# Optimization experiments

Hardware: AMD Instinct MI355X
Metric: run time of the kernel (lower is better)

Reference implementation:

```python
import jax, jax.numpy as jnp
import numpy as np

S, N, LAT, HID, NH, NLAYERS = 8, 128, 128, 384, 8, 6
HT, WT, DT = 128, 128, 128
DIN, DOUT, RAD, LEVELS, FED = 1169, 3 + 3 * 128, 3, 4, 64


def sincos1d(d, pos):
    # MAE-style 1d sincos embedding, d even -> [..., d]
    omega = 1.0 / (10000.0 ** (jnp.arange(d // 2, dtype=jnp.float32) / (d / 2.0)))
    ang = pos[..., None] * omega
    return jnp.concatenate([jnp.sin(ang), jnp.cos(ang)], axis=-1)


def flow_embed(f, Cd=FED):
    # get_3d_embedding(flows, 64, cat_coords=True) -> [..., 3*Cd+3] = 195
    div = jnp.arange(0, Cd, 2, dtype=jnp.float32) * (1000.0 / Cd)
    outs = []
    for a in range(3):
        ang = f[..., a, None] * div
        pe = jnp.stack([jnp.sin(ang), jnp.cos(ang)], axis=-1).reshape(f.shape[:-1] + (Cd,))
        outs.append(pe)
    return jnp.concatenate(outs + [f], axis=-1)


def avg_pool2(x):
    B, Sv, Cc, H, W = x.shape
    return x.reshape(B, Sv, Cc, H // 2, 2, W // 2, 2).mean(axis=(4, 6))


def pyramid(fm):
    pyr = [fm]
    for _ in range(LEVELS - 1):
        fm = avg_pool2(fm)
        pyr.append(fm)
    return pyr


def bilinear_sample(corr, xy):
    # corr: [B,S,N,H,W]; xy: [B,S,N,P,2] pixel coords (x indexes W, y indexes H); zero padding
    B, Sv, Nn, H, W = corr.shape
    cf = corr.reshape(B, Sv, Nn, H * W)
    x, y = xy[..., 0], xy[..., 1]
    x0f = jnp.floor(x); y0f = jnp.floor(y)
    wx, wy = x - x0f, y - y0f
    x0 = x0f.astype(jnp.int32); y0 = y0f.astype(jnp.int32)

    def gather(xi, yi):
        ok = ((xi >= 0) & (xi < W) & (yi >= 0) & (yi < H)).astype(cf.dtype)
        idx = jnp.clip(yi, 0, H - 1) * W + jnp.clip(xi, 0, W - 1)
        v = jnp.take_along_axis(cf, idx.reshape(B, Sv, Nn, -1), axis=-1).reshape(idx.shape)
        return v * ok

    v00 = gather(x0, y0); v01 = gather(x0 + 1, y0)
    v10 = gather(x0, y0 + 1); v11 = gather(x0 + 1, y0 + 1)
    return v00 * (1 - wx) * (1 - wy) + v01 * wx * (1 - wy) + v10 * (1 - wx) * wy + v11 * wx * wy


def corr_sample(pyr, targets, coords):
    # RAFT/CoTracker CorrBlock: per-level dense correlation then (2r+1)^2 window bilinear lookup
    d = jnp.arange(-RAD, RAD + 1, dtype=jnp.float32)
    delta = jnp.stack(jnp.meshgrid(d, d, indexing="ij"), axis=-1).reshape(-1, 2)  # [49,2]
    scale = 1.0 / jnp.sqrt(jnp.float32(targets.shape[-1]))
    outs = []
    for l, fm in enumerate(pyr):
        corr = jnp.einsum("bsnc,bschw->bsnhw", targets, fm) * scale
        xy = coords[..., None, :] / (2.0 ** l) + delta
        outs.append(bilinear_sample(corr, xy))
    return jnp.concatenate(outs, axis=-1)  # [B,S,N,196]


def layernorm(x, g, b):
    m = x.mean(-1, keepdims=True)
    v = x.var(-1, keepdims=True)
    return (x - m) / jnp.sqrt(v + 1e-5) * g + b


def attention(x, Wqkv, bq, Wo, bo):
    M, T, H = x.shape
    dh = H // NH
    qkv = (x @ Wqkv + bq).reshape(M, T, 3, NH, dh)
    q, k, v = qkv[:, :, 0], qkv[:, :, 1], qkv[:, :, 2]
    att = jax.nn.softmax(jnp.einsum("mthd,mshd->mhts", q, k) / jnp.sqrt(jnp.float32(dh)), axis=-1)
    o = jnp.einsum("mhts,mshd->mthd", att, v).reshape(M, T, H)
    return o @ Wo + bo


def updateformer(x, support, W_in, b_in, lnp, Wqkv, bqkv, Wo, bo, W1, b1, W2, b2, W_out, b_out, Ws, bs):
    # x: [B,N,T,DIN]; alternating time (over T) and space (over N) pre-LN transformer blocks
    B, Np, T, _ = x.shape
    sproj = support @ Ws + bs  # [100,HID]
    h = x @ W_in + b_in + sproj.mean(axis=0)
    for i in range(NLAYERS):
        g1, bb1, g2, bb2 = lnp[i, 0], lnp[i, 1], lnp[i, 2], lnp[i, 3]
        if i % 2 == 0:
            y = h.reshape(B * Np, T, HID)
        else:
            y = h.transpose(0, 2, 1, 3).reshape(B * T, Np, HID)
        y = y + attention(layernorm(y, g1, bb1), Wqkv[i], bqkv[i], Wo[i], bo[i])
        z = layernorm(y, g2, bb2)
        y = y + jax.nn.gelu(z @ W1[i] + b1[i], approximate=False) @ W2[i] + b2[i]
        if i % 2 == 0:
            h = y.reshape(B, Np, T, HID)
        else:
            h = y.reshape(B, T, Np, HID).transpose(0, 2, 1, 3)
    return h @ W_out + b_out, sproj[None]


def groupnorm1(x, g, b):
    m = x.mean(-1, keepdims=True)
    v = x.var(-1, keepdims=True)
    return (x - m) / jnp.sqrt(v + 1e-5) * g + b


def _forward(fmapXY, fmapYZ, fmapXZ, coords_init, vis_init, track_mask, feat_init, support_features,
             W_in, b_in, lnp, Wqkv, bqkv, Wo, bo, W1, b1, W2, b2, W_out, b_out, Ws, bs,
             gn_g, gn_b, Wu, bu, Wvis, bvis, iters):
    B, Sv, Cc, H, W = fmapXY.shape
    D = fmapXZ.shape[-2]
    Nn = coords_init.shape[2]
    coords = coords_init
    ffeats = [feat_init[..., k] for k in range(3)]
    pyrXY, pyrYZ, pyrXZ = pyramid(fmapXY), pyramid(fmapYZ), pyramid(fmapXZ)
    grid_size = jnp.array([H, W, D], dtype=jnp.float32)
    # 3d sincos pos embed from query coords; 1169 padded to 1170 -> 390/axis, truncated back
    g = (coords[:, 0] / grid_size * 2.0 - 1.0) * 128.0  # [B,N,3]
    pe = jnp.concatenate([sincos1d(390, g[..., i]) for i in range(3)], axis=-1)[..., :DIN]
    pos_embed = pe.reshape(B * Nn, 1, DIN)
    times_embed = sincos1d(1170, jnp.arange(Sv, dtype=jnp.float32))[None, :, :DIN]
    support = support_features
    for _ in range(iters):
        coords = jax.lax.stop_gradient(coords)  # matches coords.detach()
        fxy = corr_sample(pyrXY, ffeats[0], coords[..., :2])
        fyz = corr_sample(pyrYZ, ffeats[1], coords[..., 1:3])
        fxz = corr_sample(pyrXZ, ffeats[2], coords[..., 0::2])
        fcorrs = jnp.concatenate([fxy, fyz, fxz], axis=-1)  # [B,S,N,588]
        fcorrs_ = fcorrs.transpose(0, 2, 1, 3).reshape(B * Nn, Sv, -1)
        flows_ = (coords - coords[:, :1]).transpose(0, 2, 1, 3).reshape(B * Nn, Sv, 3)
        flows_cat = flow_embed(flows_)  # [BN,S,195]
        ff = [f.transpose(0, 2, 1, 3).reshape(B * Nn, Sv, LAT) for f in ffeats]
        ffeats_ = jnp.concatenate(ff, axis=-1)  # [BN,S,384]
        # replicate torch's cat(dim=2)+permute+reshape layout exactly
        tmv = jnp.concatenate([track_mask, vis_init], axis=2).transpose(0, 2, 1, 3).reshape(B * Nn, Sv, 2)
        tin = jnp.concatenate([flows_cat, fcorrs_, ffeats_, tmv], axis=-1)  # [BN,S,1169]
        x = (tin + pos_embed + times_embed).reshape(B, Nn, Sv, DIN)
        delta, dse3 = updateformer(x, support, W_in, b_in, lnp, Wqkv, bqkv, Wo, bo, W1, b1, W2, b2, W_out, b_out, Ws, bs)
        support = support + dse3[0] / 100.0
        delta = delta.reshape(B * Nn, Sv, DOUT)
        d_coord = delta[..., :3].reshape(B, Nn, Sv, 3).transpose(0, 2, 1, 3)
        coords = coords + d_coord
        new_ffeats = []
        for k in range(3):
            dfk = delta[..., 3 + k * LAT:3 + (k + 1) * LAT]
            upd = jax.nn.gelu(groupnorm1(dfk, gn_g[k], gn_b[k]) @ Wu[k] + bu[k], approximate=False)
            new_ffeats.append(ffeats[k] + upd.reshape(B, Nn, Sv, LAT).transpose(0, 2, 1, 3))
        ffeats = new_ffeats
    vis = (jnp.concatenate(ffeats, axis=-1) @ Wvis + bvis)[..., 0]  # [B,S,N]
    return jnp.concatenate([coords, vis[..., None]], axis=-1)  # [B,S,N,4]


def setup_inputs() -> dict:
    key = jax.random.key(0)
    ks = jax.random.split(key, 16)
    f32 = jnp.float32
    B = 1
    fmapXY = jax.random.normal(ks[0], (B, S, LAT, HT, WT), f32)
    fmapYZ = jax.random.normal(ks[1], (B, S, LAT, DT, HT), f32)
    fmapXZ = jax.random.normal(ks[2], (B, S, LAT, DT, WT), f32)
    coords_init = jax.random.uniform(ks[3], (B, S, N, 3), f32) * 112.0 + 8.0
    vis_init = jnp.ones((B, S, N, 1), f32)
    track_mask = jnp.ones((B, S, N, 1), f32)
    feat_init = jax.random.normal(ks[4], (B, S, N, LAT, 3), f32)
    support_features = jnp.zeros((100, HID), f32) + 0.1
    w = lambda k, sh: jax.random.normal(k, sh, f32) * 0.02
    ln1 = jnp.stack([jnp.ones(HID, f32), jnp.zeros(HID, f32), jnp.ones(HID, f32), jnp.zeros(HID, f32)])
    params = dict(
        W_in=w(ks[5], (DIN, HID)), b_in=jnp.zeros((HID,), f32),
        lnp=jnp.tile(ln1[None], (NLAYERS, 1, 1)),
        Wqkv=w(ks[6], (NLAYERS, HID, 3 * HID)), bqkv=jnp.zeros((NLAYERS, 3 * HID), f32),
        Wo=w(ks[7], (NLAYERS, HID, HID)), bo=jnp.zeros((NLAYERS, HID), f32),
        W1=w(ks[8], (NLAYERS, HID, 4 * HID)), b1=jnp.zeros((NLAYERS, 4 * HID), f32),
        W2=w(ks[9], (NLAYERS, 4 * HID, HID)), b2=jnp.zeros((NLAYERS, HID), f32),
        W_out=w(ks[10], (HID, DOUT)), b_out=jnp.zeros((DOUT,), f32),
        Ws=w(ks[11], (HID, HID)), bs=jnp.zeros((HID,), f32),
        gn_g=jnp.ones((3, LAT), f32), gn_b=jnp.zeros((3, LAT), f32),
        Wu=w(ks[12], (3, LAT, LAT)), bu=jnp.zeros((3, LAT), f32),
        Wvis=w(ks[13], (3 * LAT, 1)), bvis=jnp.zeros((1,), f32),
    )
    return dict(fmapXY=fmapXY, fmapYZ=fmapYZ, fmapXZ=fmapXZ, coords_init=coords_init,
                vis_init=vis_init, track_mask=track_mask, feat_init=feat_init,
                support_features=support_features, iters=2, **params)


def reference(fmapXY, fmapYZ, fmapXZ, coords_init, vis_init, track_mask, feat_init, support_features,
              W_in, b_in, lnp, Wqkv, bqkv, Wo, bo, W1, b1, W2, b2, W_out, b_out, Ws, bs,
              gn_g, gn_b, Wu, bu, Wvis, bvis, iters):
    return _forward(fmapXY, fmapYZ, fmapXZ, coords_init, vis_init, track_mask, feat_init, support_features,
                    W_in, b_in, lnp, Wqkv, bqkv, Wo, bo, W1, b1, W2, b2, W_out, b_out, Ws, bs,
                    gn_g, gn_b, Wu, bu, Wvis, bvis, iters)
```

## Files before the change

kernel.cpp:

```cpp
#include <hip/hip_runtime.h>
#include <hip/hip_bf16.h>


#define DEVFN __device__ __forceinline__

typedef __attribute__((ext_vector_type(8))) short short8;
typedef __attribute__((ext_vector_type(4))) float f32x4;

static constexpr float INV_SQRT_DH = 0.14433756729740643f;
static constexpr float CORR_SCALE  = 0.08838834764831845f;
static constexpr size_t VSTRIDE = 22282240;

DEVFN float gelu_exact(float x){
  return 0.5f * x * (1.0f + erff(x * 0.7071067811865476f));
}
DEVFN short bf16_of(float f){
  __hip_bfloat16 b = __float2bfloat16(f);
  return *reinterpret_cast<short*>(&b);
}
DEVFN float bfu(uint32_t u16){ return __uint_as_float(u16 << 16); }


__global__ void init_state_k(float* coords, const float* cinit,
                             float* ff, const float* feat_init,
                             float* support, const float* sfeat){
  int idx = blockIdx.x*256 + threadIdx.x;
  if (idx < 3072)  coords[idx]  = cinit[idx];
  if (idx < 49152){
    int row = idx / 384;
    support[idx] = (row < 100) ? sfeat[idx] : 0.0f;
  }
  if (idx < 393216){
    int k = idx / 131072, rest = idx % 131072;
    ff[idx] = feat_init[(size_t)rest*3 + k];
  }
}

__global__ void build_posE_k(float* posE, const float* cinit){
  int idx = blockIdx.x*256 + threadIdx.x;
  if (idx >= 128*1169) return;
  int n = idx / 1169, d = idx % 1169;
  int i = d / 390, dd = d % 390;
  float c = cinit[n*3 + i];
  float g = (c / 128.0f * 2.0f - 1.0f) * 128.0f;
  int m = (dd < 195) ? dd : dd - 195;
  float om = powf(10000.0f, -(float)m / 195.0f);
  float ang = g * om;
  posE[idx] = (dd < 195) ? sinf(ang) : cosf(ang);
}

__global__ void build_timE_k(float* timE){
  int idx = blockIdx.x*256 + threadIdx.x;
  if (idx >= 8*1169) return;
  int s = idx / 1169, d = idx % 1169;
  int m = (d < 585) ? d : d - 585;
  float om = powf(10000.0f, -(float)m / 585.0f);
  float ang = (float)s * om;
  timE[idx] = (d < 585) ? sinf(ang) : cosf(ang);
}

__global__ void transpose_cl_k(const float* __restrict__ inXY, const float* __restrict__ inYZ,
                               const float* __restrict__ inXZ, __hip_bfloat16* __restrict__ pyr){
  __shared__ float tile[32][33];
  int v = blockIdx.z >> 3, s = blockIdx.z & 7;
  const float* in = (v==0) ? inXY : ((v==1) ? inYZ : inXZ);
  int c0 = blockIdx.y*32, h0 = blockIdx.x*32;
  int tx = threadIdx.x & 31, ty = threadIdx.x >> 5;
  const float* ib = in + (size_t)s*128*16384;
  #pragma unroll
  for (int r=0;r<4;r++){
    int c = c0 + ty + r*8;
    tile[ty + r*8][tx] = ib[(size_t)c*16384 + h0 + tx];
  }
  __syncthreads();
  __hip_bfloat16* ob = pyr + (size_t)v*VSTRIDE + (size_t)s*16384*128;
  #pragma unroll
  for (int r=0;r<4;r++){
    int hw = h0 + ty + r*8;
    ob[(size_t)hw*128 + c0 + tx] = __float2bfloat16(tile[tx][ty + r*8]);
  }
}

__global__ void pool2_k(__hip_bfloat16* __restrict__ pyr, size_t in_off, size_t out_off, int So){
  int idx = blockIdx.x*256 + threadIdx.x;
  int total = 8*So*So*128;
  if (idx >= total) return;
  const __hip_bfloat16* in = pyr + (size_t)blockIdx.z*VSTRIDE + in_off;
  __hip_bfloat16* out      = pyr + (size_t)blockIdx.z*VSTRIDE + out_off;
  int c = idx & 127;
  int x = (idx >> 7) % So;
  int y = ((idx >> 7) / So) % So;
  int s = idx / (So*So*128);
  int Si = So*2;
  const __hip_bfloat16* b0 = in + (((size_t)s*Si + 2*y)*Si + 2*x)*128 + c;
  float v = __bfloat162float(b0[0]) + __bfloat162float(b0[128])
          + __bfloat162float(b0[(size_t)Si*128]) + __bfloat162float(b0[(size_t)Si*128 + 128]);
  out[idx] = __float2bfloat16(v*0.25f);
}

__global__ void wtrans_k(const float* __restrict__ in, __hip_bfloat16* __restrict__ out,
                         int K, int N, int Kpad, int Npad){
  __shared__ float tile[32][33];
  int z = blockIdx.z;
  const float* ib = in + (size_t)z*K*N;
  __hip_bfloat16* ob = out + (size_t)z*Npad*Kpad;
  int kb = blockIdx.y*32, nb = blockIdx.x*32;
  int tx = threadIdx.x & 31, ty = threadIdx.x >> 5;
  #pragma unroll
  for (int r=0;r<4;r++){
    int k = kb + ty + r*8, n = nb + tx;
    tile[ty+r*8][tx] = (k < K && n < N) ? ib[(size_t)k*N + n] : 0.0f;
  }
  __syncthreads();
  #pragma unroll
  for (int r=0;r<4;r++){
    int n = nb + ty + r*8, k = kb + tx;
    if (n < Npad && k < Kpad) ob[(size_t)n*Kpad + k] = __float2bfloat16(tile[tx][ty+r*8]);
  }
}

__global__ void assemble_x_k(__hip_bfloat16* __restrict__ xbuf, const float* __restrict__ posE,
                             const float* __restrict__ timE, const float* __restrict__ coords,
                             const float* __restrict__ ff, const float* __restrict__ tmask,
                             const float* __restrict__ vinit){
  int r = blockIdx.x;
  int n = r >> 3, s = r & 7;
  for (int d = threadIdx.x; d < 1184; d += blockDim.x){
    __hip_bfloat16* dst = xbuf + (size_t)r*1184 + d;
    if (d >= 1169){ *dst = __float2bfloat16(0.0f); continue; }
    float base = posE[(size_t)n*1169 + d] + timE[(size_t)s*1169 + d];
    if (d >= 195 && d < 783){ *dst = __float2bfloat16(base); continue; }
    float val;
    if (d < 195){
      if (d >= 192){
        int a = d - 192;
        val = coords[(s*128+n)*3 + a] - coords[n*3 + a];
      } else {
        int a = d >> 6, dd = d & 63;
        float f = coords[(s*128+n)*3 + a] - coords[n*3 + a];
        float ang = f * (31.25f * (float)(dd >> 1));
        val = (dd & 1) ? cosf(ang) : sinf(ang);
      }
    } else if (d < 1167){
      int cidx = d - 783, k = cidx >> 7, cc = cidx & 127;
      val = ff[(size_t)k*131072 + (size_t)(s*128+n)*128 + cc];
    } else {
      int c = d - 1167;
      int flat = n*16 + s*2 + c;
      int n2 = flat >> 3, s2 = flat & 7;
      val = (n2 < 128) ? tmask[s2*128 + n2] : vinit[s2*128 + (n2-128)];
    }
    *dst = __float2bfloat16(val + base);
  }
}

__global__ void corr_k(const __hip_bfloat16* __restrict__ pyr, const float* __restrict__ coords,
                       const float* __restrict__ ff, __hip_bfloat16* __restrict__ xbuf){
  __shared__ float t[128];
  __shared__ float p[64];
  int bid = blockIdx.x;
  int view = bid >> 10, s = (bid >> 7) & 7, n = bid & 127;
  int tid = threadIdx.x;
  t[tid]      = ff[(size_t)view*131072 + (size_t)(s*128+n)*128 + tid];
  t[tid + 64] = ff[(size_t)view*131072 + (size_t)(s*128+n)*128 + tid + 64];
  int ax = (view==1) ? 1 : 0;
  int ay = (view==0) ? 1 : 2;
  float X = coords[(s*128+n)*3 + ax];
  float Y = coords[(s*128+n)*3 + ay];
  const __hip_bfloat16* vb = pyr + (size_t)view*VSTRIDE;
  __syncthreads();
  size_t loff = 0;
  for (int l=0;l<4;l++){
    int sz = 128 >> l;
    float inv = 1.0f / (float)(1 << l);
    float cx = X * inv, cy = Y * inv;
    float x0f = floorf(cx), y0f = floorf(cy);
    float wx = cx - x0f, wy = cy - y0f;
    int ix0 = (int)x0f, iy0 = (int)y0f;
    int px = ix0 - 3 + (tid & 7);
    int py = iy0 - 3 + (tid >> 3);
    float acc = 0.0f;
    if (px >= 0 && px < sz && py >= 0 && py < sz){
      const uint2* row = reinterpret_cast<const uint2*>(vb + loff + (((size_t)s*sz + py)*sz + px)*128);
      #pragma unroll
      for (int c4=0;c4<32;c4++){
        uint2 u = row[c4];
        float f0 = __uint_as_float(u.x << 16);
        float f1 = __uint_as_float(u.x & 0xffff0000u);
        float f2 = __uint_as_float(u.y << 16);
        float f3 = __uint_as_float(u.y & 0xffff0000u);
        acc += t[c4*4+0]*f0 + t[c4*4+1]*f1 + t[c4*4+2]*f2 + t[c4*4+3]*f3;
      }
    }
    p[tid] = acc;
    __syncthreads();
    if (tid < 49){
      int i = tid / 7, jj = tid % 7;
      float v = p[jj*8+i]       * (1.0f-wx)*(1.0f-wy)
              + p[jj*8+i+1]     * wx*(1.0f-wy)
              + p[(jj+1)*8+i]   * (1.0f-wx)*wy
              + p[(jj+1)*8+i+1] * wx*wy;
      __hip_bfloat16* dst = xbuf + (size_t)(n*8+s)*1184 + 195 + view*196 + l*49 + tid;
      *dst = __float2bfloat16(__bfloat162float(*dst) + v * CORR_SCALE);
    }
    loff += (size_t)8*sz*sz*128;
    __syncthreads();
  }
}

__global__ void gn_rows_k(const float* __restrict__ dbuf,
                          const float* __restrict__ gn_g, const float* __restrict__ gn_b,
                          __hip_bfloat16* __restrict__ gtmp, float* __restrict__ coords){
  int k = blockIdx.y;
  const float* in = dbuf + 3 + k*128;
  const float* g = gn_g + k*128;
  const float* b = gn_b + k*128;
  __hip_bfloat16* out = gtmp + (size_t)k*131072;
  int wave = threadIdx.x >> 6, lane = threadIdx.x & 63;
  int r = blockIdx.x*4 + wave;
  const float* row = in + (size_t)r*387;
  float x0 = row[lane], x1 = row[lane+64];
  float sum = x0 + x1;
  #pragma unroll
  for (int o=32;o>0;o>>=1) sum += __shfl_xor(sum, o);
  float mean = sum / 128.0f;
  float d0 = x0-mean, d1 = x1-mean;
  float vs = d0*d0 + d1*d1;
  #pragma unroll
  for (int o=32;o>0;o>>=1) vs += __shfl_xor(vs, o);
  float invstd = 1.0f / sqrtf(vs/128.0f + 1e-5f);
  out[(size_t)r*128 + lane]      = __float2bfloat16(d0*invstd*g[lane] + b[lane]);
  out[(size_t)r*128 + lane + 64] = __float2bfloat16(d1*invstd*g[lane+64] + b[lane+64]);
  if (k == 0 && blockIdx.x < 12){
    int idx = blockIdx.x*256 + threadIdx.x;
    if (idx < 3072){
      int a = idx % 3, sn = idx / 3;
      int ss = sn >> 7, nn = sn & 127;
      coords[idx] += dbuf[(size_t)(nn*8+ss)*387 + a];
    }
  }
}

template<int K, int MODE, bool AF32>
__global__ __launch_bounds__(256) void mgemm_k(const void* __restrict__ A, int lda,
                                               const __hip_bfloat16* __restrict__ Bt,
                                               float* __restrict__ C, int ldc,
                                               int M, int N,
                                               const float* __restrict__ bias){
  constexpr int NSTEP = K/32;
  int tid = threadIdx.x;
  int lane = tid & 63, wid = tid >> 6;
  int wr = wid >> 1, wc = wid & 1;
  int lr = lane & 15, lk = lane >> 4;
  int m0 = blockIdx.y*64 + wr*32;
  int n0 = blockIdx.x*64 + wc*32;

  const __hip_bfloat16* Ab = (const __hip_bfloat16*)A;
  const float* Af = (const float*)A;
  size_t arow0 = (size_t)(m0 + lr)      * lda;
  size_t arow1 = (size_t)(m0 + 16 + lr) * lda;
  size_t brow0 = (size_t)(n0 + lr)      * K;
  size_t brow1 = (size_t)(n0 + 16 + lr) * K;

  auto loadA = [&](size_t ro, int k0)->short8{
    if constexpr (AF32){
      const float* p = Af + ro + k0 + lk*8;
      short8 r;
      #pragma unroll
      for (int j=0;j<8;j++) r[j] = bf16_of(p[j]);
      return r;
    } else {
      return *reinterpret_cast<const short8*>(Ab + ro + k0 + lk*8);
    }
  };
  auto loadB = [&](size_t ro, int k0)->short8{
    return *reinterpret_cast<const short8*>(Bt + ro + k0 + lk*8);
  };

  short8 a0[3], a1[3], b0[3], b1[3];
  #pragma unroll
  for (int p=0;p<3;p++){
    if (p < NSTEP){
      a0[p]=loadA(arow0,p*32); a1[p]=loadA(arow1,p*32);
      b0[p]=loadB(brow0,p*32); b1[p]=loadB(brow1,p*32);
    }
  }
  f32x4 acc00 = {}, acc01 = {}, acc10 = {}, acc11 = {};
  #pragma unroll
  for (int t=0;t<NSTEP;t++){
    const int cur = t % 3;
    acc00 = __builtin_amdgcn_mfma_f32_16x16x32_bf16(a0[cur],b0[cur],acc00,0,0,0);
    acc01 = __builtin_amdgcn_mfma_f32_16x16x32_bf16(a0[cur],b1[cur],acc01,0,0,0);
    acc10 = __builtin_amdgcn_mfma_f32_16x16x32_bf16(a1[cur],b0[cur],acc10,0,0,0);
    acc11 = __builtin_amdgcn_mfma_f32_16x16x32_bf16(a1[cur],b1[cur],acc11,0,0,0);
    if (t+3 < NSTEP){
      int k0 = (t+3)*32;
      a0[cur]=loadA(arow0,k0); a1[cur]=loadA(arow1,k0);
      b0[cur]=loadB(brow0,k0); b1[cur]=loadB(brow1,k0);
    }
  }

  f32x4 accs[2][2] = {{acc00, acc01},{acc10, acc11}};
  #pragma unroll
  for (int mi=0;mi<2;mi++){
    #pragma unroll
    for (int ni=0;ni<2;ni++){
      int c = n0 + ni*16 + lr;
      if (c >= N) continue;
      float bv = bias ? bias[c] : 0.0f;
      #pragma unroll
      for (int reg=0;reg<4;reg++){
        int r = m0 + mi*16 + lk*4 + reg;
        if (r >= M) continue;
        float v = accs[mi][ni][reg] + bv;
        if (MODE==0) C[(size_t)r*ldc + c] = v;
        else C[(size_t)r*ldc + c] += v;
      }
    }
  }
}

template<bool GELU>
__global__ __launch_bounds__(256) void lngemm_k(const float* __restrict__ A,
                                                const float* __restrict__ gamma,
                                                const float* __restrict__ beta,
                                                const __hip_bfloat16* __restrict__ Bt,
                                                __hip_bfloat16* __restrict__ Cbf, int ldc,
                                                const float* __restrict__ bias){
  constexpr int LDSS = 392;
  __shared__ short Asm[64*LDSS];
  int tid = threadIdx.x, lane = tid & 63, w = tid >> 6;
  int m0 = blockIdx.y*64, n0b = blockIdx.x*128;

  float gg[6], bb[6];
  #pragma unroll
  for (int e=0;e<6;e++){ gg[e] = gamma[lane+e*64]; bb[e] = beta[lane+e*64]; }
  for (int rr=0; rr<16; rr++){
    int r = w*16 + rr;
    const float* row = A + (size_t)(m0+r)*384;
    float x[6]; float sum = 0.0f;
    #pragma unroll
    for (int e=0;e<6;e++){ x[e] = row[lane+e*64]; sum += x[e]; }
    #pragma unroll
    for (int o=32;o>0;o>>=1) sum += __shfl_xor(sum, o);
    float mean = sum * (1.0f/384.0f);
    float vs = 0.0f;
    #pragma unroll
    for (int e=0;e<6;e++){ float d = x[e]-mean; vs += d*d; }
    #pragma unroll
    for (int o=32;o>0;o>>=1) vs += __shfl_xor(vs, o);
    float invstd = 1.0f / sqrtf(vs*(1.0f/384.0f) + 1e-5f);
    #pragma unroll
    for (int e=0;e<6;e++)
      Asm[r*LDSS + lane + e*64] = bf16_of((x[e]-mean)*invstd*gg[e] + bb[e]);
  }
  __syncthreads();

  int wr = w >> 1, wc = w & 1;
  int lr = lane & 15, lk = lane >> 4;
  const __hip_bfloat16* Brow[4];
  #pragma unroll
  for (int ni=0;ni<4;ni++) Brow[ni] = Bt + (size_t)(n0b + wc*64 + ni*16 + lr)*384;

  short8 bfrag[2][4];
  #pragma unroll
  for (int p=0;p<2;p++)
    #pragma unroll
    for (int ni=0;ni<4;ni++)
      bfrag[p][ni] = *(const short8*)(Brow[ni] + p*32 + lk*8);

  f32x4 acc[2][4] = {};
  #pragma unroll
  for (int t=0;t<12;t++){
    const int cur = t & 1;
    short8 a0 = *(const short8*)(&Asm[(wr*32+lr)*LDSS    + t*32 + lk*8]);
    short8 a1 = *(const short8*)(&Asm[(wr*32+16+lr)*LDSS + t*32 + lk*8]);
    #pragma unroll
    for (int ni=0;ni<4;ni++){
      acc[0][ni] = __builtin_amdgcn_mfma_f32_16x16x32_bf16(a0,bfrag[cur][ni],acc[0][ni],0,0,0);
      acc[1][ni] = __builtin_amdgcn_mfma_f32_16x16x32_bf16(a1,bfrag[cur][ni],acc[1][ni],0,0,0);
    }
    if (t+2 < 12){
      #pragma unroll
      for (int ni=0;ni<4;ni++)
        bfrag[cur][ni] = *(const short8*)(Brow[ni] + (t+2)*32 + lk*8);
    }
  }
  #pragma unroll
  for (int mi=0;mi<2;mi++){
    #pragma unroll
    for (int ni=0;ni<4;ni++){
      int c = n0b + wc*64 + ni*16 + lr;
      float bv = bias[c];
      #pragma unroll
      for (int reg=0;reg<4;reg++){
        int r = m0 + wr*32 + mi*16 + lk*4 + reg;
        float v = acc[mi][ni][reg] + bv;
        Cbf[(size_t)r*ldc + c] = __float2bfloat16(GELU ? gelu_exact(v) : v);
      }
    }
  }
}

__global__ __launch_bounds__(256) void wu_gemm_k(const __hip_bfloat16* __restrict__ gtmp,
                                                 const __hip_bfloat16* __restrict__ WuT,
                                                 const float* __restrict__ bu,
                                                 float* __restrict__ ff){
  int z = blockIdx.z;
  const __hip_bfloat16* A  = gtmp + (size_t)z*131072;
  const __hip_bfloat16* Bt = WuT  + (size_t)z*16384;
  const float* bias = bu + (size_t)z*128;
  float* aux = ff + (size_t)z*131072;
  int tid = threadIdx.x, lane = tid & 63, wid = tid >> 6;
  int wr = wid >> 1, wc = wid & 1;
  int lr = lane & 15, lk = lane >> 4;
  int m0 = blockIdx.y*64 + wr*32;
  int n0 = blockIdx.x*64 + wc*32;
  const short8* A0 = (const short8*)(A + (size_t)(m0+lr)*128);
  const short8* A1 = (const short8*)(A + (size_t)(m0+16+lr)*128);
  const short8* B0 = (const short8*)(Bt + (size_t)(n0+lr)*128);
  const short8* B1 = (const short8*)(Bt + (size_t)(n0+16+lr)*128);
  f32x4 acc00={}, acc01={}, acc10={}, acc11={};
  #pragma unroll
  for (int t=0;t<4;t++){
    short8 a0 = A0[t*4 + lk], a1 = A1[t*4 + lk];
    short8 b0 = B0[t*4 + lk], b1 = B1[t*4 + lk];
    acc00 = __builtin_amdgcn_mfma_f32_16x16x32_bf16(a0,b0,acc00,0,0,0);
    acc01 = __builtin_amdgcn_mfma_f32_16x16x32_bf16(a0,b1,acc01,0,0,0);
    acc10 = __builtin_amdgcn_mfma_f32_16x16x32_bf16(a1,b0,acc10,0,0,0);
    acc11 = __builtin_amdgcn_mfma_f32_16x16x32_bf16(a1,b1,acc11,0,0,0);
  }
  f32x4 accs[2][2] = {{acc00, acc01},{acc10, acc11}};
  #pragma unroll
  for (int mi=0;mi<2;mi++){
    #pragma unroll
    for (int ni=0;ni<2;ni++){
      int c = n0 + ni*16 + lr;
      float bv = bias[c];
      #pragma unroll
      for (int reg=0;reg<4;reg++){
        int r = m0 + mi*16 + lk*4 + reg;
        float v = accs[mi][ni][reg] + bv;
        int ss = r & 7, nn2 = r >> 3;
        aux[((size_t)(ss*128+nn2))*128 + c] += gelu_exact(v);
      }
    }
  }
}

__global__ __launch_bounds__(512) void attn_even_k(const __hip_bfloat16* __restrict__ qkv,
                                                   __hip_bfloat16* __restrict__ attout){
  int g = blockIdx.x;
  int h = threadIdx.x >> 6;
  int lane = threadIdx.x & 63;
  int t = lane >> 3, j = lane & 7;
  const short* qs = (const short*)qkv;

  float q[48], kk[48];
  {
    const short8* qp = (const short8*)(qs + (size_t)(g*8+t)*1152 + h*48);
    const short8* kp = (const short8*)(qs + (size_t)(g*8+j)*1152 + 384 + h*48);
    #pragma unroll
    for (int c=0;c<6;c++){
      short8 qv = qp[c], kv = kp[c];
      #pragma unroll
      for (int e=0;e<8;e++){
        q[c*8+e]  = bfu((uint16_t)qv[e]);
        kk[c*8+e] = bfu((uint16_t)kv[e]);
      }
    }
  }
  float s = 0.0f;
  #pragma unroll
  for (int d=0;d<48;d++) s += q[d]*kk[d];
  s *= INV_SQRT_DH;
  float mx = s;
  #pragma unroll
  for (int o=1;o<8;o<<=1) mx = fmaxf(mx, __shfl_xor(mx, o));
  float e = expf(s - mx);
  float l = e;
  #pragma unroll
  for (int o=1;o<8;o<<=1) l += __shfl_xor(l, o);
  float p = e / l;

  float o6[6] = {0,0,0,0,0,0};
  #pragma unroll
  for (int jp=0;jp<8;jp++){
    float pj = __shfl(p, (lane & 56) | jp);
    const uint32_t* vp = (const uint32_t*)(qs + (size_t)(g*8+jp)*1152 + 768 + h*48 + j*6);
    uint32_t w0 = vp[0], w1 = vp[1], w2 = vp[2];
    o6[0] += pj * bfu(w0 & 0xffffu); o6[1] += pj * bfu(w0 >> 16);
    o6[2] += pj * bfu(w1 & 0xffffu); o6[3] += pj * bfu(w1 >> 16);
    o6[4] += pj * bfu(w2 & 0xffffu); o6[5] += pj * bfu(w2 >> 16);
  }
  uint32_t r0 = ((uint32_t)(uint16_t)bf16_of(o6[1]) << 16) | (uint16_t)bf16_of(o6[0]);
  uint32_t r1 = ((uint32_t)(uint16_t)bf16_of(o6[3]) << 16) | (uint16_t)bf16_of(o6[2]);
  uint32_t r2 = ((uint32_t)(uint16_t)bf16_of(o6[5]) << 16) | (uint16_t)bf16_of(o6[4]);
  uint32_t* op = (uint32_t*)((short*)attout + (size_t)(g*8+t)*384 + h*48 + j*6);
  op[0] = r0; op[1] = r1; op[2] = r2;
}

__global__ __launch_bounds__(256) void attn_odd_mfma_k(const __hip_bfloat16* __restrict__ qkv,
                                                       __hip_bfloat16* __restrict__ attout){
  __shared__ char smem[47872];
  short* Qb = (short*)smem;
  short* Kb = (short*)(smem + 18432);
  short* Pb = (short*)smem;
  short* Vt = (short*)(smem + 34816);
  int g = blockIdx.x & 7, h = blockIdx.x >> 3;
  int tid = threadIdx.x;

  const short* qs = (const short*)qkv;
  for (int idx = tid; idx < 768; idx += 256){
    int t = idx / 6, dblk = idx % 6;
    size_t base = (size_t)(t*8+g)*1152 + h*48 + dblk*8;
    *(short8*)(Qb + t*72 + dblk*8) = *(const short8*)(qs + base);
    *(short8*)(Kb + t*72 + dblk*8) = *(const short8*)(qs + base + 384);
  }
  short8 zz = {};
  for (int idx = tid; idx < 384; idx += 256){
    int t = idx / 3, dblk = idx % 3;
    *(short8*)(Qb + t*72 + 48 + dblk*8) = zz;
    *(short8*)(Kb + t*72 + 48 + dblk*8) = zz;
  }
  __syncthreads();

  int lane = tid & 63, w = tid >> 6;
  int lr = lane & 15, lk = lane >> 4;
  int m0 = w*32;

  f32x4 S[2][8] = {};
  #pragma unroll
  for (int ks=0; ks<2; ks++){
    short8 a0 = *(const short8*)(Qb + (m0+lr)*72    + ks*32 + lk*8);
    short8 a1 = *(const short8*)(Qb + (m0+16+lr)*72 + ks*32 + lk*8);
    #pragma unroll
    for (int ni=0; ni<8; ni++){
      short8 b = *(const short8*)(Kb + (ni*16+lr)*72 + ks*32 + lk*8);
      S[0][ni] = __builtin_amdgcn_mfma_f32_16x16x32_bf16(a0,b,S[0][ni],0,0,0);
      S[1][ni] = __builtin_amdgcn_mfma_f32_16x16x32_bf16(a1,b,S[1][ni],0,0,0);
    }
  }

  #pragma unroll
  for (int mi=0;mi<2;mi++){
    #pragma unroll
    for (int reg=0;reg<4;reg++){
      float m = -1e30f;
      #pragma unroll
      for (int ni=0;ni<8;ni++) m = fmaxf(m, S[mi][ni][reg]);
      #pragma unroll
      for (int o=1;o<16;o<<=1) m = fmaxf(m, __shfl_xor(m, o));
      m *= INV_SQRT_DH;
      float l = 0.0f;
      #pragma unroll
      for (int ni=0;ni<8;ni++){
        float p = expf(S[mi][ni][reg]*INV_SQRT_DH - m);
        S[mi][ni][reg] = p;
        l += p;
      }
      #pragma unroll
      for (int o=1;o<16;o<<=1) l += __shfl_xor(l, o);
      float inv = 1.0f/l;
      #pragma unroll
      for (int ni=0;ni<8;ni++) S[mi][ni][reg] *= inv;
    }
  }
  __syncthreads();

  for (int idx = tid; idx < 768; idx += 256){
    int j = idx / 6, dblk = idx % 6;
    short8 v = *(const short8*)(qs + (size_t)(j*8+g)*1152 + 768 + h*48 + dblk*8);
    #pragma unroll
    for (int e=0;e<8;e++) Vt[(dblk*8+e)*136 + j] = v[e];
  }
  #pragma unroll
  for (int mi=0;mi<2;mi++)
    #pragma unroll
    for (int ni=0;ni<8;ni++)
      #pragma unroll
      for (int reg=0;reg<4;reg++)
        Pb[(m0+mi*16+lk*4+reg)*136 + ni*16+lr] = bf16_of(S[mi][ni][reg]);
  __syncthreads();

  f32x4 O[2][3] = {};
  #pragma unroll
  for (int ks=0; ks<4; ks++){
    short8 a0 = *(const short8*)(Pb + (m0+lr)*136    + ks*32 + lk*8);
    short8 a1 = *(const short8*)(Pb + (m0+16+lr)*136 + ks*32 + lk*8);
    #pragma unroll
    for (int ni=0; ni<3; ni++){
      short8 b = *(const short8*)(Vt + (ni*16+lr)*136 + ks*32 + lk*8);
      O[0][ni] = __builtin_amdgcn_mfma_f32_16x16x32_bf16(a0,b,O[0][ni],0,0,0);
      O[1][ni] = __builtin_amdgcn_mfma_f32_16x16x32_bf16(a1,b,O[1][ni],0,0,0);
    }
  }
  #pragma unroll
  for (int mi=0;mi<2;mi++){
    #pragma unroll
    for (int ni=0;ni<3;ni++){
      #pragma unroll
      for (int reg=0;reg<4;reg++){
        int q = m0 + mi*16 + lk*4 + reg;
        int d = ni*16 + lr;
        attout[(size_t)(q*8+g)*384 + h*48 + d] = __float2bfloat16(O[mi][ni][reg]);
      }
    }
  }
}

__global__ void supp_smean_k(const float* __restrict__ sproj, const float* __restrict__ b_in,
                             float* __restrict__ bias2, float* __restrict__ support){
  int idx = blockIdx.x*256 + threadIdx.x;
  if (idx < 38400) support[idx] += sproj[idx]*0.01f;
  else if (idx < 38784){
    int c = idx - 38400;
    float s = 0.0f;
    for (int r=0;r<100;r++) s += sproj[r*384 + c];
    bias2[c] = b_in[c] + s*0.01f;
  }
}

__global__ void final_out_k(const float* __restrict__ coords, const float* __restrict__ ff,
                            const float* __restrict__ Wvis, const float* __restrict__ bvis,
                            float* __restrict__ out){
  int sn = blockIdx.x*64 + threadIdx.x;
  if (sn >= 1024) return;
  float acc = bvis[0];
  for (int k=0;k<3;k++)
    for (int c=0;c<128;c++)
      acc += ff[(size_t)k*131072 + (size_t)sn*128 + c] * Wvis[k*128 + c];
  out[sn*4+0] = coords[sn*3+0];
  out[sn*4+1] = coords[sn*3+1];
  out[sn*4+2] = coords[sn*3+2];
  out[sn*4+3] = acc;
}


extern "C" void kernel_launch(void* const* d_in, const int* in_sizes, int n_in,
                              void* d_out, int out_size, void* d_ws, size_t ws_size,
                              hipStream_t stream) {
  const float* fmapXY   = (const float*)d_in[0];
  const float* fmapYZ   = (const float*)d_in[1];
  const float* fmapXZ   = (const float*)d_in[2];
  const float* cinit    = (const float*)d_in[3];
  const float* vinit    = (const float*)d_in[4];
  const float* tmask    = (const float*)d_in[5];
  const float* feat_init= (const float*)d_in[6];
  const float* sfeat    = (const float*)d_in[7];
  const float* W_in     = (const float*)d_in[9];
  const float* b_in     = (const float*)d_in[10];
  const float* lnp      = (const float*)d_in[11];
  const float* Wqkv     = (const float*)d_in[12];
  const float* bqkv     = (const float*)d_in[13];
  const float* Wo       = (const float*)d_in[14];
  const float* bo       = (const float*)d_in[15];
  const float* W1       = (const float*)d_in[16];
  const float* b1       = (const float*)d_in[17];
  const float* W2       = (const float*)d_in[18];
  const float* b2       = (const float*)d_in[19];
  const float* W_out    = (const float*)d_in[20];
  const float* b_out    = (const float*)d_in[21];
  const float* Ws       = (const float*)d_in[22];
  const float* bs       = (const float*)d_in[23];
  const float* gn_g     = (const float*)d_in[24];
  const float* gn_b     = (const float*)d_in[25];
  const float* Wu       = (const float*)d_in[26];
  const float* bu       = (const float*)d_in[27];
  const float* Wvis     = (const float*)d_in[28];
  const float* bvis     = (const float*)d_in[29];
  const int ITERS = 2;

  char* wp = (char*)d_ws;
  auto alloc = [&](size_t bytes)->char* {
    char* p = wp; wp += (bytes + 255) & ~(size_t)255; return p;
  };
  __hip_bfloat16* pyr = (__hip_bfloat16*)alloc(3ull*VSTRIDE*2);
  float* coords = (float*)alloc(3072ull*4);
  float* ff     = (float*)alloc(393216ull*4);
  float* support= (float*)alloc(49152ull*4);
  float* sproj  = (float*)alloc(38400ull*4);
  float* bias2  = (float*)alloc(384ull*4);
  float* posE   = (float*)alloc(149632ull*4);
  float* timE   = (float*)alloc(9352ull*4);
  float* h      = (float*)alloc(393216ull*4);
  float* dbuf   = (float*)alloc(396288ull*4);
  __hip_bfloat16* xbuf_bf = (__hip_bfloat16*)alloc(1212416ull*2);
  __hip_bfloat16* qkv_bf  = (__hip_bfloat16*)alloc(1179648ull*2);
  __hip_bfloat16* atto_bf = (__hip_bfloat16*)alloc(393216ull*2);
  __hip_bfloat16* ffb_bf  = (__hip_bfloat16*)alloc(1572864ull*2);
  __hip_bfloat16* gtmp_bf = (__hip_bfloat16*)alloc(393216ull*2);
  __hip_bfloat16* WsT   = (__hip_bfloat16*)alloc(147456ull*2);
  __hip_bfloat16* WinT  = (__hip_bfloat16*)alloc(454656ull*2);
  __hip_bfloat16* WqkvT = (__hip_bfloat16*)alloc(2654208ull*2);
  __hip_bfloat16* WoT   = (__hip_bfloat16*)alloc(884736ull*2);
  __hip_bfloat16* W1T   = (__hip_bfloat16*)alloc(3538944ull*2);
  __hip_bfloat16* W2T   = (__hip_bfloat16*)alloc(3538944ull*2);
  __hip_bfloat16* WoutT = (__hip_bfloat16*)alloc(172032ull*2);
  __hip_bfloat16* WuT   = (__hip_bfloat16*)alloc(49152ull*2);
  if ((size_t)(wp - (char*)d_ws) > ws_size) return;

  init_state_k<<<1536, 256, 0, stream>>>(coords, cinit, ff, feat_init, support, sfeat);
  build_posE_k<<<(128*1169 + 255)/256, 256, 0, stream>>>(posE, cinit);
  build_timE_k<<<(8*1169 + 255)/256, 256, 0, stream>>>(timE);

  transpose_cl_k<<<dim3(512,4,24), 256, 0, stream>>>(fmapXY, fmapYZ, fmapXZ, pyr);
  pool2_k<<<dim3((8*64*64*128 + 255)/256,1,3), 256, 0, stream>>>(pyr, 0,        16777216, 64);
  pool2_k<<<dim3((8*32*32*128 + 255)/256,1,3), 256, 0, stream>>>(pyr, 16777216, 20971520, 32);
  pool2_k<<<dim3((8*16*16*128 + 255)/256,1,3), 256, 0, stream>>>(pyr, 20971520, 22020096, 16);

  wtrans_k<<<dim3(12,12,1), 256, 0, stream>>>(Ws,    WsT,   384, 384, 384, 384);
  wtrans_k<<<dim3(12,37,1), 256, 0, stream>>>(W_in,  WinT,  1169,384, 1184,384);
  wtrans_k<<<dim3(36,12,6), 256, 0, stream>>>(Wqkv,  WqkvT, 384, 1152,384, 1152);
  wtrans_k<<<dim3(12,12,6), 256, 0, stream>>>(Wo,    WoT,   384, 384, 384, 384);
  wtrans_k<<<dim3(48,12,6), 256, 0, stream>>>(W1,    W1T,   384, 1536,384, 1536);
  wtrans_k<<<dim3(12,48,6), 256, 0, stream>>>(W2,    W2T,   1536,384, 1536,384);
  wtrans_k<<<dim3(14,12,1), 256, 0, stream>>>(W_out, WoutT, 384, 387, 384, 448);
  wtrans_k<<<dim3(4,4,3),   256, 0, stream>>>(Wu,    WuT,   128, 128, 128, 128);

  for (int it=0; it<ITERS; ++it){
    assemble_x_k<<<1024, 256, 0, stream>>>(xbuf_bf, posE, timE, coords, ff, tmask, vinit);
    corr_k<<<3072, 64, 0, stream>>>(pyr, coords, ff, xbuf_bf);

    mgemm_k<384,0,true><<<dim3(6,2), 256, 0, stream>>>(support,384, WsT, sproj,384, 100,384, bs);
    supp_smean_k<<<152, 256, 0, stream>>>(sproj, b_in, bias2, support);

    mgemm_k<1184,0,false><<<dim3(6,16), 256, 0, stream>>>(xbuf_bf,1184, WinT, h,384, 1024,384, bias2);

    for (int i=0;i<6;i++){
      const float* g1  = lnp + (size_t)(i*4+0)*384;
      const float* bb1 = lnp + (size_t)(i*4+1)*384;
      const float* g2  = lnp + (size_t)(i*4+2)*384;
      const float* bb2 = lnp + (size_t)(i*4+3)*384;

      lngemm_k<false><<<dim3(9,16), 256, 0, stream>>>(h, g1, bb1, WqkvT + (size_t)i*442368,
                                                      qkv_bf, 1152, bqkv + i*1152);
      if ((i & 1) == 0) attn_even_k<<<128, 512, 0, stream>>>(qkv_bf, atto_bf);
      else              attn_odd_mfma_k<<<64, 256, 0, stream>>>(qkv_bf, atto_bf);
      mgemm_k<384,1,false><<<dim3(6,16), 256, 0, stream>>>(atto_bf,384, WoT + (size_t)i*147456,
                                                           h,384, 1024,384, bo + i*384);
      lngemm_k<true><<<dim3(12,16), 256, 0, stream>>>(h, g2, bb2, W1T + (size_t)i*589824,
                                                      ffb_bf, 1536, b1 + i*1536);
      mgemm_k<1536,1,false><<<dim3(6,16), 256, 0, stream>>>(ffb_bf,1536, W2T + (size_t)i*589824,
                                                            h,384, 1024,384, b2 + i*384);
    }

    mgemm_k<384,0,true><<<dim3(7,16), 256, 0, stream>>>(h,384, WoutT, dbuf,387, 1024,387, b_out);
    gn_rows_k<<<dim3(256,3), 256, 0, stream>>>(dbuf, gn_g, gn_b, gtmp_bf, coords);
    wu_gemm_k<<<dim3(2,16,3), 256, 0, stream>>>(gtmp_bf, WuT, bu, ff);
  }

  final_out_k<<<16, 64, 0, stream>>>(coords, ff, Wvis, bvis, (float*)d_out);
}
```

Measured before the change: 1.459 ms.

## Fuse setup kernels, Wo+LN+W1, and output head; deepen GEMM prefetch

Merges the init, positional-embedding, pooling and weight-transpose launches into single kernels. The pyramid pooling now reads level 0 directly for every level, and the transpose tile is widened to use float4 loads. Per layer, the Wo projection, residual add, LayerNorm and W1 GELU GEMM become one kernel with ping-pong h buffers, and the output head, GroupNorm and Wu update are fused. Prefetch depth rises in mgemm and the LN GEMMs. These changes cut launch count and round-trips through global memory, but each W1 block recomputes the full Wo GEMM for its row tile, and the coarser pooling reads more data.

After: 2.211 ms. +51.6%, slower.

```diff
diff --git a/kernel.cpp b/kernel.cpp
--- a/kernel.cpp
+++ b/kernel.cpp
@@ -19,11 +19,16 @@
   return *reinterpret_cast<short*>(&b);
 }
 DEVFN float bfu(uint32_t u16){ return __uint_as_float(u16 << 16); }
-
-
-__global__ void init_state_k(float* coords, const float* cinit,
-                             float* ff, const float* feat_init,
-                             float* support, const float* sfeat){
+DEVFN float bf2f(__hip_bfloat16 b){ return __bfloat162float(b); }
+
+DEVFN f32x4 MFMA(short8 a, short8 b, f32x4 c){
+  return __builtin_amdgcn_mfma_f32_16x16x32_bf16(a,b,c,0,0,0);
+}
+
+__global__ void init_all_k(float* coords, const float* cinit,
+                           float* ff, const float* feat_init,
+                           float* support, const float* sfeat,
+                           float* posE, float* timE){
   int idx = blockIdx.x*256 + threadIdx.x;
   if (idx < 3072)  coords[idx]  = cinit[idx];
   if (idx < 49152){
@@ -34,88 +39,99 @@
     int k = idx / 131072, rest = idx % 131072;
     ff[idx] = feat_init[(size_t)rest*3 + k];
   }
-}
-
-__global__ void build_posE_k(float* posE, const float* cinit){
-  int idx = blockIdx.x*256 + threadIdx.x;
-  if (idx >= 128*1169) return;
-  int n = idx / 1169, d = idx % 1169;
-  int i = d / 390, dd = d % 390;
-  float c = cinit[n*3 + i];
-  float g = (c / 128.0f * 2.0f - 1.0f) * 128.0f;
-  int m = (dd < 195) ? dd : dd - 195;
-  float om = powf(10000.0f, -(float)m / 195.0f);
-  float ang = g * om;
-  posE[idx] = (dd < 195) ? sinf(ang) : cosf(ang);
-}
-
-__global__ void build_timE_k(float* timE){
-  int idx = blockIdx.x*256 + threadIdx.x;
-  if (idx >= 8*1169) return;
-  int s = idx / 1169, d = idx % 1169;
-  int m = (d < 585) ? d : d - 585;
-  float om = powf(10000.0f, -(float)m / 585.0f);
-  float ang = (float)s * om;
-  timE[idx] = (d < 585) ? sinf(ang) : cosf(ang);
+  if (idx < 149632){
+    int n = idx / 1169, d = idx % 1169;
+    int i = d / 390, dd = d % 390;
+    float c = cinit[n*3 + i];
+    float g = (c / 128.0f * 2.0f - 1.0f) * 128.0f;
+    int m = (dd < 195) ? dd : dd - 195;
+    float om = powf(10000.0f, -(float)m / 195.0f);
+    float ang = g * om;
+    posE[idx] = (dd < 195) ? sinf(ang) : cosf(ang);
+  }
+  if (idx < 9352){
+    int s = idx / 1169, d = idx % 1169;
+    int m = (d < 585) ? d : d - 585;
+    float om = powf(10000.0f, -(float)m / 585.0f);
+    float ang = (float)s * om;
+    timE[idx] = (d < 585) ? sinf(ang) : cosf(ang);
+  }
 }
 
 __global__ void transpose_cl_k(const float* __restrict__ inXY, const float* __restrict__ inYZ,
                                const float* __restrict__ inXZ, __hip_bfloat16* __restrict__ pyr){
-  __shared__ float tile[32][33];
+  __shared__ float tile[32][129];
   int v = blockIdx.z >> 3, s = blockIdx.z & 7;
   const float* in = (v==0) ? inXY : ((v==1) ? inYZ : inXZ);
-  int c0 = blockIdx.y*32, h0 = blockIdx.x*32;
+  int c0 = blockIdx.y*32, h0 = blockIdx.x*128;
   int tx = threadIdx.x & 31, ty = threadIdx.x >> 5;
   const float* ib = in + (size_t)s*128*16384;
   #pragma unroll
   for (int r=0;r<4;r++){
     int c = c0 + ty + r*8;
-    tile[ty + r*8][tx] = ib[(size_t)c*16384 + h0 + tx];
+    float4 f = *reinterpret_cast<const float4*>(ib + (size_t)c*16384 + h0 + tx*4);
+    tile[ty+r*8][tx*4+0]=f.x; tile[ty+r*8][tx*4+1]=f.y;
+    tile[ty+r*8][tx*4+2]=f.z; tile[ty+r*8][tx*4+3]=f.w;
   }
   __syncthreads();
   __hip_bfloat16* ob = pyr + (size_t)v*VSTRIDE + (size_t)s*16384*128;
   #pragma unroll
-  for (int r=0;r<4;r++){
-    int hw = h0 + ty + r*8;
-    ob[(size_t)hw*128 + c0 + tx] = __float2bfloat16(tile[tx][ty + r*8]);
-  }
-}
-
-__global__ void pool2_k(__hip_bfloat16* __restrict__ pyr, size_t in_off, size_t out_off, int So){
+  for (int rr=0;rr<16;rr++){
+    int hw = ty + rr*8;
+    ob[(size_t)(h0+hw)*128 + c0 + tx] = __float2bfloat16(tile[tx][hw]);
+  }
+}
+
+__global__ void pool_all_k(__hip_bfloat16* __restrict__ pyr){
   int idx = blockIdx.x*256 + threadIdx.x;
-  int total = 8*So*So*128;
-  if (idx >= total) return;
-  const __hip_bfloat16* in = pyr + (size_t)blockIdx.z*VSTRIDE + in_off;
-  __hip_bfloat16* out      = pyr + (size_t)blockIdx.z*VSTRIDE + out_off;
-  int c = idx & 127;
-  int x = (idx >> 7) % So;
-  int y = ((idx >> 7) / So) % So;
-  int s = idx / (So*So*128);
-  int Si = So*2;
-  const __hip_bfloat16* b0 = in + (((size_t)s*Si + 2*y)*Si + 2*x)*128 + c;
-  float v = __bfloat162float(b0[0]) + __bfloat162float(b0[128])
-          + __bfloat162float(b0[(size_t)Si*128]) + __bfloat162float(b0[(size_t)Si*128 + 128]);
-  out[idx] = __float2bfloat16(v*0.25f);
-}
-
-__global__ void wtrans_k(const float* __restrict__ in, __hip_bfloat16* __restrict__ out,
-                         int K, int N, int Kpad, int Npad){
+  if (idx >= 5505024) return;
+  const __hip_bfloat16* L0 = pyr + (size_t)blockIdx.z*VSTRIDE;
+  int i = idx, So, F; size_t off;
+  if (i < 4194304){ So=64; F=2; off=16777216; }
+  else if (i < 5242880){ i -= 4194304; So=32; F=4; off=20971520; }
+  else { i -= 5242880; So=16; F=8; off=22020096; }
+  int c = i & 127;
+  int x = (i >> 7) % So;
+  int y = ((i >> 7) / So) % So;
+  int s = i / (So*So*128);
+  float acc = 0.0f;
+  for (int dy=0;dy<F;dy++)
+    for (int dx=0;dx<F;dx++)
+      acc += bf2f(L0[(((size_t)s*128 + y*F+dy)*128 + (x*F+dx))*128 + c]);
+  pyr[(size_t)blockIdx.z*VSTRIDE + off + i] = __float2bfloat16(acc / (float)(F*F));
+}
+
+__global__ void wtrans_all_k(const float* Ws, const float* W_in, const float* Wqkv,
+                             const float* Wo, const float* W1, const float* W2,
+                             const float* W_out, const float* Wu,
+                             __hip_bfloat16* WsT, __hip_bfloat16* WinT, __hip_bfloat16* WqkvT,
+                             __hip_bfloat16* WoT, __hip_bfloat16* W1T, __hip_bfloat16* W2T,
+                             __hip_bfloat16* WoutT, __hip_bfloat16* WuT){
   __shared__ float tile[32][33];
   int z = blockIdx.z;
-  const float* ib = in + (size_t)z*K*N;
-  __hip_bfloat16* ob = out + (size_t)z*Npad*Kpad;
+  const float* in; __hip_bfloat16* out; int K,N,Kp,Np;
+  if (z==0){ in=Ws; out=WsT; K=384;N=384;Kp=384;Np=384; }
+  else if (z==1){ in=W_in; out=WinT; K=1169;N=384;Kp=1184;Np=384; }
+  else if (z<8){ int l=z-2; in=Wqkv+(size_t)l*442368; out=WqkvT+(size_t)l*442368; K=384;N=1152;Kp=384;Np=1152; }
+  else if (z<14){ int l=z-8; in=Wo+(size_t)l*147456; out=WoT+(size_t)l*147456; K=384;N=384;Kp=384;Np=384; }
+  else if (z<20){ int l=z-14; in=W1+(size_t)l*589824; out=W1T+(size_t)l*589824; K=384;N=1536;Kp=384;Np=1536; }
+  else if (z<26){ int l=z-20; in=W2+(size_t)l*589824; out=W2T+(size_t)l*589824; K=1536;N=384;Kp=1536;Np=384; }
+  else if (z==26){ in=W_out; out=WoutT; K=384;N=387;Kp=384;Np=448; }
+  else { int l=z-27; in=Wu+(size_t)l*16384; out=WuT+(size_t)l*16384; K=128;N=128;Kp=128;Np=128; }
+  int MK = (K>Kp)?K:Kp, MN = (N>Np)?N:Np;
   int kb = blockIdx.y*32, nb = blockIdx.x*32;
+  if (kb >= MK || nb >= MN) return;
   int tx = threadIdx.x & 31, ty = threadIdx.x >> 5;
   #pragma unroll
   for (int r=0;r<4;r++){
     int k = kb + ty + r*8, n = nb + tx;
-    tile[ty+r*8][tx] = (k < K && n < N) ? ib[(size_t)k*N + n] : 0.0f;
+    tile[ty+r*8][tx] = (k < K && n < N) ? in[(size_t)k*N + n] : 0.0f;
   }
   __syncthreads();
   #pragma unroll
   for (int r=0;r<4;r++){
     int n = nb + ty + r*8, k = kb + tx;
-    if (n < Npad && k < Kpad) ob[(size_t)n*Kpad + k] = __float2bfloat16(tile[tx][ty+r*8]);
+    if (n < Np && k < Kp) out[(size_t)n*Kp + k] = __float2bfloat16(tile[tx][ty+r*8]);
   }
 }
 
@@ -208,40 +224,7 @@
   }
 }
 
-__global__ void gn_rows_k(const float* __restrict__ dbuf,
-                          const float* __restrict__ gn_g, const float* __restrict__ gn_b,
-                          __hip_bfloat16* __restrict__ gtmp, float* __restrict__ coords){
-  int k = blockIdx.y;
-  const float* in = dbuf + 3 + k*128;
-  const float* g = gn_g + k*128;
-  const float* b = gn_b + k*128;
-  __hip_bfloat16* out = gtmp + (size_t)k*131072;
-  int wave = threadIdx.x >> 6, lane = threadIdx.x & 63;
-  int r = blockIdx.x*4 + wave;
-  const float* row = in + (size_t)r*387;
-  float x0 = row[lane], x1 = row[lane+64];
-  float sum = x0 + x1;
-  #pragma unroll
-  for (int o=32;o>0;o>>=1) sum += __shfl_xor(sum, o);
-  float mean = sum / 128.0f;
-  float d0 = x0-mean, d1 = x1-mean;
-  float vs = d0*d0 + d1*d1;
-  #pragma unroll
-  for (int o=32;o>0;o>>=1) vs += __shfl_xor(vs, o);
-  float invstd = 1.0f / sqrtf(vs/128.0f + 1e-5f);
-  out[(size_t)r*128 + lane]      = __float2bfloat16(d0*invstd*g[lane] + b[lane]);
-  out[(size_t)r*128 + lane + 64] = __float2bfloat16(d1*invstd*g[lane+64] + b[lane+64]);
-  if (k == 0 && blockIdx.x < 12){
-    int idx = blockIdx.x*256 + threadIdx.x;
-    if (idx < 3072){
-      int a = idx % 3, sn = idx / 3;
-      int ss = sn >> 7, nn = sn & 127;
-      coords[idx] += dbuf[(size_t)(nn*8+ss)*387 + a];
-    }
-  }
-}
-
-template<int K, int MODE, bool AF32>
+template<int K, int MODE, bool AF32, int DEPTH>
 __global__ __launch_bounds__(256) void mgemm_k(const void* __restrict__ A, int lda,
                                                const __hip_bfloat16* __restrict__ Bt,
                                                float* __restrict__ C, int ldc,
@@ -277,9 +260,9 @@
     return *reinterpret_cast<const short8*>(Bt + ro + k0 + lk*8);
   };
 
-  short8 a0[3], a1[3], b0[3], b1[3];
-  #pragma unroll
-  for (int p=0;p<3;p++){
+  short8 a0[DEPTH], a1[DEPTH], b0[DEPTH], b1[DEPTH];
+  #pragma unroll
+  for (int p=0;p<DEPTH;p++){
     if (p < NSTEP){
       a0[p]=loadA(arow0,p*32); a1[p]=loadA(arow1,p*32);
       b0[p]=loadB(brow0,p*32); b1[p]=loadB(brow1,p*32);
@@ -288,13 +271,13 @@
   f32x4 acc00 = {}, acc01 = {}, acc10 = {}, acc11 = {};
   #pragma unroll
   for (int t=0;t<NSTEP;t++){
-    const int cur = t % 3;
-    acc00 = __builtin_amdgcn_mfma_f32_16x16x32_bf16(a0[cur],b0[cur],acc00,0,0,0);
-    acc01 = __builtin_amdgcn_mfma_f32_16x16x32_bf16(a0[cur],b1[cur],acc01,0,0,0);
-    acc10 = __builtin_amdgcn_mfma_f32_16x16x32_bf16(a1[cur],b0[cur],acc10,0,0,0);
-    acc11 = __builtin_amdgcn_mfma_f32_16x16x32_bf16(a1[cur],b1[cur],acc11,0,0,0);
-    if (t+3 < NSTEP){
-      int k0 = (t+3)*32;
+    const int cur = t % DEPTH;
+    acc00 = MFMA(a0[cur],b0[cur],acc00);
+    acc01 = MFMA(a0[cur],b1[cur],acc01);
+    acc10 = MFMA(a1[cur],b0[cur],acc10);
+    acc11 = MFMA(a1[cur],b1[cur],acc11);
+    if (t+DEPTH < NSTEP){
+      int k0 = (t+DEPTH)*32;
       a0[cur]=loadA(arow0,k0); a1[cur]=loadA(arow1,k0);
       b0[cur]=loadB(brow0,k0); b1[cur]=loadB(brow1,k0);
     }
@@ -320,12 +303,11 @@
   }
 }
 
-template<bool GELU>
-__global__ __launch_bounds__(256) void lngemm_k(const float* __restrict__ A,
+__global__ __launch_bounds__(256) void ln_qkv_k(const float* __restrict__ A,
                                                 const float* __restrict__ gamma,
                                                 const float* __restrict__ beta,
                                                 const __hip_bfloat16* __restrict__ Bt,
-                                                __hip_bfloat16* __restrict__ Cbf, int ldc,
+                                                __hip_bfloat16* __restrict__ Cbf,
                                                 const float* __restrict__ bias){
   constexpr int LDSS = 392;
   __shared__ short Asm[64*LDSS];
@@ -362,9 +344,9 @@
   #pragma unroll
   for (int ni=0;ni<4;ni++) Brow[ni] = Bt + (size_t)(n0b + wc*64 + ni*16 + lr)*384;
 
-  short8 bfrag[2][4];
-  #pragma unroll
-  for (int p=0;p<2;p++)
+  short8 bfrag[4][4];
+  #pragma unroll
+  for (int p=0;p<4;p++)
     #pragma unroll
     for (int ni=0;ni<4;ni++)
       bfrag[p][ni] = *(const short8*)(Brow[ni] + p*32 + lk*8);
@@ -372,18 +354,18 @@
   f32x4 acc[2][4] = {};
   #pragma unroll
   for (int t=0;t<12;t++){
-    const int cur = t & 1;
+    const int cur = t & 3;
     short8 a0 = *(const short8*)(&Asm[(wr*32+lr)*LDSS    + t*32 + lk*8]);
     short8 a1 = *(const short8*)(&Asm[(wr*32+16+lr)*LDSS + t*32 + lk*8]);
     #pragma unroll
     for (int ni=0;ni<4;ni++){
-      acc[0][ni] = __builtin_amdgcn_mfma_f32_16x16x32_bf16(a0,bfrag[cur][ni],acc[0][ni],0,0,0);
-      acc[1][ni] = __builtin_amdgcn_mfma_f32_16x16x32_bf16(a1,bfrag[cur][ni],acc[1][ni],0,0,0);
-    }
-    if (t+2 < 12){
+      acc[0][ni] = MFMA(a0,bfrag[cur][ni],acc[0][ni]);
+      acc[1][ni] = MFMA(a1,bfrag[cur][ni],acc[1][ni]);
+    }
+    if (t+4 < 12){
       #pragma unroll
       for (int ni=0;ni<4;ni++)
-        bfrag[cur][ni] = *(const short8*)(Brow[ni] + (t+2)*32 + lk*8);
+        bfrag[cur][ni] = *(const short8*)(Brow[ni] + (t+4)*32 + lk*8);
     }
   }
   #pragma unroll
@@ -395,52 +377,235 @@
       #pragma unroll
       for (int reg=0;reg<4;reg++){
         int r = m0 + wr*32 + mi*16 + lk*4 + reg;
-        float v = acc[mi][ni][reg] + bv;
-        Cbf[(size_t)r*ldc + c] = __float2bfloat16(GELU ? gelu_exact(v) : v);
+        Cbf[(size_t)r*1152 + c] = __float2bfloat16(acc[mi][ni][reg] + bv);
       }
     }
   }
 }
 
-__global__ __launch_bounds__(256) void wu_gemm_k(const __hip_bfloat16* __restrict__ gtmp,
-                                                 const __hip_bfloat16* __restrict__ WuT,
-                                                 const float* __restrict__ bu,
-                                                 float* __restrict__ ff){
-  int z = blockIdx.z;
-  const __hip_bfloat16* A  = gtmp + (size_t)z*131072;
-  const __hip_bfloat16* Bt = WuT  + (size_t)z*16384;
-  const float* bias = bu + (size_t)z*128;
+__global__ __launch_bounds__(256) void wo_ln_w1_k(const __hip_bfloat16* __restrict__ atto,
+                                                  const __hip_bfloat16* __restrict__ WoT,
+                                                  const float* __restrict__ bo,
+                                                  const float* __restrict__ hin,
+                                                  float* __restrict__ hout,
+                                                  const float* __restrict__ gamma,
+                                                  const float* __restrict__ beta,
+                                                  const __hip_bfloat16* __restrict__ W1T,
+                                                  const float* __restrict__ b1,
+                                                  __hip_bfloat16* __restrict__ ffb){
+  constexpr int LDSS = 392;
+  __shared__ short Asm[64*LDSS];
+  int tid = threadIdx.x, lane = tid & 63, w = tid >> 6;
+  int lr = lane & 15, lk = lane >> 4;
+  int m0 = blockIdx.y*64;
+
+  f32x4 acc[24];
+  #pragma unroll
+  for (int nt=0;nt<24;nt++) acc[nt] = (f32x4){0.f,0.f,0.f,0.f};
+  const __hip_bfloat16* Arow = atto + (size_t)(m0 + w*16 + lr)*384;
+  #pragma unroll
+  for (int t=0;t<12;t++){
+    short8 a = *(const short8*)(Arow + t*32 + lk*8);
+    #pragma unroll
+    for (int nt=0;nt<24;nt++){
+      short8 b = *(const short8*)(WoT + (size_t)(nt*16+lr)*384 + t*32 + lk*8);
+      acc[nt] = MFMA(a,b,acc[nt]);
+    }
+  }
+  int rbase = m0 + w*16 + lk*4;
+  float sum[4] = {0,0,0,0}, sq[4] = {0,0,0,0};
+  #pragma unroll
+  for (int nt=0;nt<24;nt++){
+    int c = nt*16 + lr;
+    float bv = bo[c];
+    #pragma unroll
+    for (int reg=0;reg<4;reg++){
+      float v = acc[nt][reg] + hin[(size_t)(rbase+reg)*384 + c] + bv;
+      acc[nt][reg] = v;
+      sum[reg] += v; sq[reg] += v*v;
+    }
+  }
+  if (blockIdx.x == 0){
+    #pragma unroll
+    for (int nt=0;nt<24;nt++){
+      int c = nt*16 + lr;
+      #pragma unroll
+      for (int reg=0;reg<4;reg++)
+        hout[(size_t)(rbase+reg)*384 + c] = acc[nt][reg];
+    }
+  }
+  #pragma unroll
+  for (int reg=0;reg<4;reg++){
+    #pragma unroll
+    for (int o=1;o<16;o<<=1){
+      sum[reg] += __shfl_xor(sum[reg], o);
+      sq[reg]  += __shfl_xor(sq[reg], o);
+    }
+  }
+  #pragma unroll
+  for (int reg=0;reg<4;reg++){
+    float mean = sum[reg]*(1.0f/384.0f);
+    float var  = sq[reg]*(1.0f/384.0f) - mean*mean;
+    float inv  = 1.0f / sqrtf(var + 1e-5f);
+    int rloc = w*16 + lk*4 + reg;
+    #pragma unroll
+    for (int nt=0;nt<24;nt++){
+      int c = nt*16 + lr;
+      Asm[rloc*LDSS + c] = bf16_of((acc[nt][reg]-mean)*inv*gamma[c] + beta[c]);
+    }
+  }
+  __syncthreads();
+
+  int wr = w >> 1, wc = w & 1;
+  int n0b = blockIdx.x*128;
+  const __hip_bfloat16* Brow[4];
+  #pragma unroll
+  for (int ni=0;ni<4;ni++) Brow[ni] = W1T + (size_t)(n0b + wc*64 + ni*16 + lr)*384;
+  short8 bfrag[4][4];
+  #pragma unroll
+  for (int p=0;p<4;p++)
+    #pragma unroll
+    for (int ni=0;ni<4;ni++)
+      bfrag[p][ni] = *(const short8*)(Brow[ni] + p*32 + lk*8);
+  f32x4 acc2[2][4] = {};
+  #pragma unroll
+  for (int t=0;t<12;t++){
+    const int cur = t & 3;
+    short8 a0 = *(const short8*)(&Asm[(wr*32+lr)*LDSS    + t*32 + lk*8]);
+    short8 a1 = *(const short8*)(&Asm[(wr*32+16+lr)*LDSS + t*32 + lk*8]);
+    #pragma unroll
+    for (int ni=0;ni<4;ni++){
+      acc2[0][ni] = MFMA(a0,bfrag[cur][ni],acc2[0][ni]);
+      acc2[1][ni] = MFMA(a1,bfrag[cur][ni],acc2[1][ni]);
+    }
+    if (t+4 < 12){
+      #pragma unroll
+      for (int ni=0;ni<4;ni++)
+        bfrag[cur][ni] = *(const short8*)(Brow[ni] + (t+4)*32 + lk*8);
+    }
+  }
+  #pragma unroll
+  for (int mi=0;mi<2;mi++){
+    #pragma unroll
+    for (int ni=0;ni<4;ni++){
+      int c = n0b + wc*64 + ni*16 + lr;
+      float bv = b1[c];
+      #pragma unroll
+      for (int reg=0;reg<4;reg++){
+        int r = m0 + wr*32 + mi*16 + lk*4 + reg;
+        ffb[(size_t)r*1536 + c] = __float2bfloat16(gelu_exact(acc2[mi][ni][reg] + bv));
+      }
+    }
+  }
+}
+
+__global__ void coords_k(float* __restrict__ coords, const float* __restrict__ h,
+                         const __hip_bfloat16* __restrict__ WoutT, const float* __restrict__ b_out){
+  int idx = blockIdx.x*64 + threadIdx.x;
+  if (idx >= 3072) return;
+  int a = idx % 3, sn = idx / 3;
+  int s = sn >> 7, n = sn & 127;
+  const float* hr = h + (size_t)(n*8+s)*384;
+  const __hip_bfloat16* wr = WoutT + (size_t)a*384;
+  float p0=0,p1=0,p2=0,p3=0;
+  for (int k=0;k<384;k+=4){
+    p0 += hr[k  ]*bf2f(wr[k  ]);
+    p1 += hr[k+1]*bf2f(wr[k+1]);
+    p2 += hr[k+2]*bf2f(wr[k+2]);
+    p3 += hr[k+3]*bf2f(wr[k+3]);
+  }
+  coords[idx] += (p0+p1)+(p2+p3) + b_out[a];
+}
+
+__global__ __launch_bounds__(256) void wout_gn_wu_k(const float* __restrict__ h,
+                                                    const __hip_bfloat16* __restrict__ WoutT,
+                                                    const float* __restrict__ b_out,
+                                                    const float* __restrict__ gn_g,
+                                                    const float* __restrict__ gn_b,
+                                                    const __hip_bfloat16* __restrict__ WuT,
+                                                    const float* __restrict__ bu,
+                                                    float* __restrict__ ff){
+  __shared__ short Asm[64*136];
+  int tid = threadIdx.x, lane = tid & 63, w = tid >> 6;
+  int lr = lane & 15, lk = lane >> 4;
+  int m0 = blockIdx.x*64;
+  int z = blockIdx.y;
+
+  f32x4 acc[8];
+  #pragma unroll
+  for (int nt=0;nt<8;nt++) acc[nt] = (f32x4){0.f,0.f,0.f,0.f};
+  const float* Arow = h + (size_t)(m0 + w*16 + lr)*384;
+  #pragma unroll
+  for (int t=0;t<12;t++){
+    short8 a;
+    const float* p = Arow + t*32 + lk*8;
+    #pragma unroll
+    for (int j=0;j<8;j++) a[j] = bf16_of(p[j]);
+    #pragma unroll
+    for (int nt=0;nt<8;nt++){
+      short8 b = *(const short8*)(WoutT + (size_t)(3 + z*128 + nt*16+lr)*384 + t*32 + lk*8);
+      acc[nt] = MFMA(a,b,acc[nt]);
+    }
+  }
+  float sum[4] = {0,0,0,0}, sq[4] = {0,0,0,0};
+  #pragma unroll
+  for (int nt=0;nt<8;nt++){
+    int cc = nt*16 + lr;
+    float bv = b_out[3 + z*128 + cc];
+    #pragma unroll
+    for (int reg=0;reg<4;reg++){
+      float v = acc[nt][reg] + bv;
+      acc[nt][reg] = v;
+      sum[reg] += v; sq[reg] += v*v;
+    }
+  }
+  #pragma unroll
+  for (int reg=0;reg<4;reg++){
+    #pragma unroll
+    for (int o=1;o<16;o<<=1){
+      sum[reg] += __shfl_xor(sum[reg], o);
+      sq[reg]  += __shfl_xor(sq[reg], o);
+    }
+  }
+  #pragma unroll
+  for (int reg=0;reg<4;reg++){
+    float mean = sum[reg]*(1.0f/128.0f);
+    float var  = sq[reg]*(1.0f/128.0f) - mean*mean;
+    float inv  = 1.0f / sqrtf(var + 1e-5f);
+    int rloc = w*16 + lk*4 + reg;
+    #pragma unroll
+    for (int nt=0;nt<8;nt++){
+      int cc = nt*16 + lr;
+      Asm[rloc*136 + cc] = bf16_of((acc[nt][reg]-mean)*inv*gn_g[z*128+cc] + gn_b[z*128+cc]);
+    }
+  }
+  __syncthreads();
+
+  int wr = w >> 1, wc = w & 1;
+  const __hip_bfloat16* Bt = WuT + (size_t)z*16384;
+  f32x4 acc2[2][4] = {};
+  #pragma unroll
+  for (int t=0;t<4;t++){
+    short8 a0 = *(const short8*)(&Asm[(wr*32+lr)*136    + t*32 + lk*8]);
+    short8 a1 = *(const short8*)(&Asm[(wr*32+16+lr)*136 + t*32 + lk*8]);
+    #pragma unroll
+    for (int ni=0;ni<4;ni++){
+      short8 b = *(const short8*)(Bt + (size_t)(wc*64 + ni*16+lr)*128 + t*32 + lk*8);
+      acc2[0][ni] = MFMA(a0,b,acc2[0][ni]);
+      acc2[1][ni] = MFMA(a1,b,acc2[1][ni]);
+    }
+  }
   float* aux = ff + (size_t)z*131072;
-  int tid = threadIdx.x, lane = tid & 63, wid = tid >> 6;
-  int wr = wid >> 1, wc = wid & 1;
-  int lr = lane & 15, lk = lane >> 4;
-  int m0 = blockIdx.y*64 + wr*32;
-  int n0 = blockIdx.x*64 + wc*32;
-  const short8* A0 = (const short8*)(A + (size_t)(m0+lr)*128);
-  const short8* A1 = (const short8*)(A + (size_t)(m0+16+lr)*128);
-  const short8* B0 = (const short8*)(Bt + (size_t)(n0+lr)*128);
-  const short8* B1 = (const short8*)(Bt + (size_t)(n0+16+lr)*128);
-  f32x4 acc00={}, acc01={}, acc10={}, acc11={};
-  #pragma unroll
-  for (int t=0;t<4;t++){
-    short8 a0 = A0[t*4 + lk], a1 = A1[t*4 + lk];
-    short8 b0 = B0[t*4 + lk], b1 = B1[t*4 + lk];
-    acc00 = __builtin_amdgcn_mfma_f32_16x16x32_bf16(a0,b0,acc00,0,0,0);
-    acc01 = __builtin_amdgcn_mfma_f32_16x16x32_bf16(a0,b1,acc01,0,0,0);
-    acc10 = __builtin_amdgcn_mfma_f32_16x16x32_bf16(a1,b0,acc10,0,0,0);
-    acc11 = __builtin_amdgcn_mfma_f32_16x16x32_bf16(a1,b1,acc11,0,0,0);
-  }
-  f32x4 accs[2][2] = {{acc00, acc01},{acc10, acc11}};
   #pragma unroll
   for (int mi=0;mi<2;mi++){
     #pragma unroll
-    for (int ni=0;ni<2;ni++){
-      int c = n0 + ni*16 + lr;
-      float bv = bias[c];
+    for (int ni=0;ni<4;ni++){
+      int c = wc*64 + ni*16 + lr;
+      float bv = bu[z*128 + c];
       #pragma unroll
       for (int reg=0;reg<4;reg++){
-        int r = m0 + mi*16 + lk*4 + reg;
-        float v = accs[mi][ni][reg] + bv;
+        int r = m0 + wr*32 + mi*16 + lk*4 + reg;
+        float v = acc2[mi][ni][reg] + bv;
         int ss = r & 7, nn2 = r >> 3;
         aux[((size_t)(ss*128+nn2))*128 + c] += gelu_exact(v);
       }
@@ -537,8 +702,8 @@
     #pragma unroll
     for (int ni=0; ni<8; ni++){
       short8 b = *(const short8*)(Kb + (ni*16+lr)*72 + ks*32 + lk*8);
-      S[0][ni] = __builtin_amdgcn_mfma_f32_16x16x32_bf16(a0,b,S[0][ni],0,0,0);
-      S[1][ni] = __builtin_amdgcn_mfma_f32_16x16x32_bf16(a1,b,S[1][ni],0,0,0);
+      S[0][ni] = MFMA(a0,b,S[0][ni]);
+      S[1][ni] = MFMA(a1,b,S[1][ni]);
     }
   }
 
@@ -591,8 +756,8 @@
     #pragma unroll
     for (int ni=0; ni<3; ni++){
       short8 b = *(const short8*)(Vt + (ni*16+lr)*136 + ks*32 + lk*8);
-      O[0][ni] = __builtin_amdgcn_mfma_f32_16x16x32_bf16(a0,b,O[0][ni],0,0,0);
-      O[1][ni] = __builtin_amdgcn_mfma_f32_16x16x32_bf16(a1,b,O[1][ni],0,0,0);
+      O[0][ni] = MFMA(a0,b,O[0][ni]);
+      O[1][ni] = MFMA(a1,b,O[1][ni]);
     }
   }
   #pragma unroll
@@ -683,13 +848,12 @@
   float* bias2  = (float*)alloc(384ull*4);
   float* posE   = (float*)alloc(149632ull*4);
   float* timE   = (float*)alloc(9352ull*4);
-  float* h      = (float*)alloc(393216ull*4);
-  float* dbuf   = (float*)alloc(396288ull*4);
+  float* h0buf  = (float*)alloc(393216ull*4);
+  float* h1buf  = (float*)alloc(393216ull*4);
   __hip_bfloat16* xbuf_bf = (__hip_bfloat16*)alloc(1212416ull*2);
   __hip_bfloat16* qkv_bf  = (__hip_bfloat16*)alloc(1179648ull*2);
   __hip_bfloat16* atto_bf = (__hip_bfloat16*)alloc(393216ull*2);
   __hip_bfloat16* ffb_bf  = (__hip_bfloat16*)alloc(1572864ull*2);
-  __hip_bfloat16* gtmp_bf = (__hip_bfloat16*)alloc(393216ull*2);
   __hip_bfloat16* WsT   = (__hip_bfloat16*)alloc(147456ull*2);
   __hip_bfloat16* WinT  = (__hip_bfloat16*)alloc(454656ull*2);
   __hip_bfloat16* WqkvT = (__hip_bfloat16*)alloc(2654208ull*2);
@@ -700,54 +864,43 @@
   __hip_bfloat16* WuT   = (__hip_bfloat16*)alloc(49152ull*2);
   if ((size_t)(wp - (char*)d_ws) > ws_size) return;
 
-  init_state_k<<<1536, 256, 0, stream>>>(coords, cinit, ff, feat_init, support, sfeat);
-  build_posE_k<<<(128*1169 + 255)/256, 256, 0, stream>>>(posE, cinit);
-  build_timE_k<<<(8*1169 + 255)/256, 256, 0, stream>>>(timE);
-
-  transpose_cl_k<<<dim3(512,4,24), 256, 0, stream>>>(fmapXY, fmapYZ, fmapXZ, pyr);
-  pool2_k<<<dim3((8*64*64*128 + 255)/256,1,3), 256, 0, stream>>>(pyr, 0,        16777216, 64);
-  pool2_k<<<dim3((8*32*32*128 + 255)/256,1,3), 256, 0, stream>>>(pyr, 16777216, 20971520, 32);
-  pool2_k<<<dim3((8*16*16*128 + 255)/256,1,3), 256, 0, stream>>>(pyr, 20971520, 22020096, 16);
-
-  wtrans_k<<<dim3(12,12,1), 256, 0, stream>>>(Ws,    WsT,   384, 384, 384, 384);
-  wtrans_k<<<dim3(12,37,1), 256, 0, stream>>>(W_in,  WinT,  1169,384, 1184,384);
-  wtrans_k<<<dim3(36,12,6), 256, 0, stream>>>(Wqkv,  WqkvT, 384, 1152,384, 1152);
-  wtrans_k<<<dim3(12,12,6), 256, 0, stream>>>(Wo,    WoT,   384, 384, 384, 384);
-  wtrans_k<<<dim3(48,12,6), 256, 0, stream>>>(W1,    W1T,   384, 1536,384, 1536);
-  wtrans_k<<<dim3(12,48,6), 256, 0, stream>>>(W2,    W2T,   1536,384, 1536,384);
-  wtrans_k<<<dim3(14,12,1), 256, 0, stream>>>(W_out, WoutT, 384, 387, 384, 448);
-  wtrans_k<<<dim3(4,4,3),   256, 0, stream>>>(Wu,    WuT,   128, 128, 128, 128);
+  init_all_k<<<1536, 256, 0, stream>>>(coords, cinit, ff, feat_init, support, sfeat, posE, timE);
+  transpose_cl_k<<<dim3(128,4,24), 256, 0, stream>>>(fmapXY, fmapYZ, fmapXZ, pyr);
+  pool_all_k<<<dim3(21504,1,3), 256, 0, stream>>>(pyr);
+  wtrans_all_k<<<dim3(48,48,30), 256, 0, stream>>>(Ws, W_in, Wqkv, Wo, W1, W2, W_out, Wu,
+                                                   WsT, WinT, WqkvT, WoT, W1T, W2T, WoutT, WuT);
 
   for (int it=0; it<ITERS; ++it){
     assemble_x_k<<<1024, 256, 0, stream>>>(xbuf_bf, posE, timE, coords, ff, tmask, vinit);
     corr_k<<<3072, 64, 0, stream>>>(pyr, coords, ff, xbuf_bf);
 
-    mgemm_k<384,0,true><<<dim3(6,2), 256, 0, stream>>>(support,384, WsT, sproj,384, 100,384, bs);
+    mgemm_k<384,0,true,3><<<dim3(6,2), 256, 0, stream>>>(support,384, WsT, sproj,384, 100,384, bs);
     supp_smean_k<<<152, 256, 0, stream>>>(sproj, b_in, bias2, support);
 
-    mgemm_k<1184,0,false><<<dim3(6,16), 256, 0, stream>>>(xbuf_bf,1184, WinT, h,384, 1024,384, bias2);
-
+    mgemm_k<1184,0,false,6><<<dim3(6,16), 256, 0, stream>>>(xbuf_bf,1184, WinT, h0buf,384, 1024,384, bias2);
+
+    float* hA = h0buf;
+    float* hB = h1buf;
     for (int i=0;i<6;i++){
       const float* g1  = lnp + (size_t)(i*4+0)*384;
       const float* bb1 = lnp + (size_t)(i*4+1)*384;
       const float* g2  = lnp + (size_t)(i*4+2)*384;
       const float* bb2 = lnp + (size_t)(i*4+3)*384;
 
-      lngemm_k<false><<<dim3(9,16), 256, 0, stream>>>(h, g1, bb1, WqkvT + (size_t)i*442368,
-                                                      qkv_bf, 1152, bqkv + i*1152);
+      ln_qkv_k<<<dim3(9,16), 256, 0, stream>>>(hA, g1, bb1, WqkvT + (size_t)i*442368,
+                                               qkv_bf, bqkv + i*1152);
       if ((i & 1) == 0) attn_even_k<<<128, 512, 0, stream>>>(qkv_bf, atto_bf);
       else              attn_odd_mfma_k<<<64, 256, 0, stream>>>(qkv_bf, atto_bf);
-      mgemm_k<384,1,false><<<dim3(6,16), 256, 0, stream>>>(atto_bf,384, WoT + (size_t)i*147456,
-                                                           h,384, 1024,384, bo + i*384);
-      lngemm_k<true><<<dim3(12,16), 256, 0, stream>>>(h, g2, bb2, W1T + (size_t)i*589824,
-                                                      ffb_bf, 1536, b1 + i*1536);
-      mgemm_k<1536,1,false><<<dim3(6,16), 256, 0, stream>>>(ffb_bf,1536, W2T + (size_t)i*589824,
-                                                            h,384, 1024,384, b2 + i*384);
-    }
-
-    mgemm_k<384,0,true><<<dim3(7,16), 256, 0, stream>>>(h,384, WoutT, dbuf,387, 1024,387, b_out);
-    gn_rows_k<<<dim3(256,3), 256, 0, stream>>>(dbuf, gn_g, gn_b, gtmp_bf, coords);
-    wu_gemm_k<<<dim3(2,16,3), 256, 0, stream>>>(gtmp_bf, WuT, bu, ff);
+      wo_ln_w1_k<<<dim3(12,16), 256, 0, stream>>>(atto_bf, WoT + (size_t)i*147456, bo + i*384,
+                                                  hA, hB, g2, bb2,
+                                                  W1T + (size_t)i*589824, b1 + i*1536, ffb_bf);
+      mgemm_k<1536,1,false,6><<<dim3(6,16), 256, 0, stream>>>(ffb_bf,1536, W2T + (size_t)i*589824,
+                                                              hB,384, 1024,384, b2 + i*384);
+      float* tmp = hA; hA = hB; hB = tmp;
+    }
+
+    coords_k<<<48, 64, 0, stream>>>(coords, hA, WoutT, b_out);
+    wout_gn_wu_k<<<dim3(16,3), 256, 0, stream>>>(hA, WoutT, b_out, gn_g, gn_b, WuT, bu, ff);
   }
 
   final_out_k<<<16, 64, 0, stream>>>(coords, ff, Wvis, bvis, (float*)d_out);
```
